# Kernel tuning notes

Measured on AMD Instinct MI355X. Metric: run time of the kernel, lower is better.

Reference implementation:

```python
import jax, jax.numpy as jnp
import numpy as np


def conv2d(x, w, pad):
    # x: [N,C,H,W], w: [O,I,kh,kw]
    return jax.lax.conv_general_dilated(
        x, w, window_strides=(1, 1), padding=[(pad, pad), (pad, pad)],
        dimension_numbers=("NCHW", "OIHW", "NCHW"))


def group_norm1(x, g, b, eps=1e-5):
    # GroupNorm(1, C): normalize over (C,H,W) per sample, per-channel affine
    mu = jnp.mean(x, axis=(1, 2, 3), keepdims=True)
    var = jnp.mean((x - mu) ** 2, axis=(1, 2, 3), keepdims=True)
    xn = (x - mu) * jax.lax.rsqrt(var + eps)
    return xn * g[None, :, None, None] + b[None, :, None, None]


def maxpool_3x3_s2(x):
    return jax.lax.reduce_window(
        x, -jnp.inf, jax.lax.max, (1, 1, 3, 3), (1, 1, 2, 2),
        ((0, 0), (0, 0), (1, 1), (1, 1)))


def hr2o_layer(x, wq, wk, wv, wo, g, b):
    # x: [N,C,H,W]; pairwise attention over the N ROIs at each (h,w)
    q = conv2d(x, wq, 1)
    k = conv2d(x, wk, 1)
    v = conv2d(x, wv, 1)
    scale = 1.0 / jnp.sqrt(jnp.asarray(x.shape[1], x.dtype))
    # torch: (q.unsqueeze(1) * k.unsqueeze(0)).sum(2) == einsum over channels
    att = jnp.einsum("nchw,mchw->nmhw", q, k) * scale  # [N,N,H,W]
    att = jax.nn.softmax(att, axis=1)                    # softmax over keys (dim=1)
    virt = jnp.einsum("nmhw,mchw->nchw", att, v)        # [N,C,H,W]
    virt = jax.nn.relu(group_norm1(virt, g, b))
    virt = conv2d(virt, wo, 1)
    return x + virt  # dropout is identity in eval mode


def setup_inputs() -> dict:
    key = jax.random.key(0)
    ks = jax.random.split(key, 12)
    N, C_R, H, W, HID, NCLS, DEPTH = 64, 1024, 16, 16, 512, 60, 2
    s = 0.02
    return {
        "bg_feats": jax.random.normal(ks[0], (C_R, H, W), jnp.float32),
        "actor_feats": jax.random.normal(ks[1], (N, C_R), jnp.float32),
        "w_conv1": jax.random.normal(ks[2], (HID, 2 * C_R, 1, 1), jnp.float32) * s,
        "w_conv2": jax.random.normal(ks[3], (HID, HID, 3, 3), jnp.float32) * s,
        "w_q": jax.random.normal(ks[4], (DEPTH, HID, HID, 3, 3), jnp.float32) * s,
        "w_k": jax.random.normal(ks[5], (DEPTH, HID, HID, 3, 3), jnp.float32) * s,
        "w_v": jax.random.normal(ks[6], (DEPTH, HID, HID, 3, 3), jnp.float32) * s,
        "w_o": jax.random.normal(ks[7], (DEPTH, HID, HID, 3, 3), jnp.float32) * s,
        "gamma": jnp.ones((DEPTH, HID), jnp.float32),
        "beta": jnp.zeros((DEPTH, HID), jnp.float32),
        "w_fc1": jax.random.normal(ks[8], (HID, C_R), jnp.float32) * s,
        "w_fc2": jax.random.normal(ks[9], (NCLS, 2 * HID), jnp.float32) * s,
    }


def reference(bg_feats, actor_feats, w_conv1, w_conv2, w_q, w_k, w_v, w_o,
              gamma, beta, w_fc1, w_fc2):
    N = actor_feats.shape[0]
    C_R, H, W = bg_feats.shape
    # bg repeated per ROI, actor features tiled over spatial dims
    bg = jnp.broadcast_to(bg_feats[None], (N, C_R, H, W))
    tiled = jnp.broadcast_to(actor_feats[:, :, None, None], (N, C_R, H, W))
    x = jnp.concatenate([bg, tiled], axis=1)           # [N, 2*C_R, H, W]
    x = jax.nn.relu(conv2d(x, w_conv1, 0))             # 1x1 -> [N,HID,H,W]
    x = jax.nn.relu(conv2d(x, w_conv2, 0))             # 3x3 pad=0 -> H-2,W-2
    x = maxpool_3x3_s2(x)                              # -> 7x7
    for d in range(w_q.shape[0]):
        x = hr2o_layer(x, w_q[d], w_k[d], w_v[d], w_o[d], gamma[d], beta[d])
    high_order = jnp.mean(x, axis=(2, 3))              # gap -> [N,HID]
    roi = jax.nn.relu(actor_feats @ w_fc1.T)           # [N,HID]
    out = jnp.concatenate([roi, high_order], axis=1) @ w_fc2.T  # [N,num_classes]
    return out
```

## Files before the change

kernel.cpp:

```cpp
#include <hip/hip_runtime.h>
#include <math.h>


typedef __bf16 bf16x8 __attribute__((ext_vector_type(8)));
typedef float  f32x4  __attribute__((ext_vector_type(4)));

#define NROI 64
#define CR   1024
#define HIDC 512
#define NCLS 60
#define PLANE (NROI * HIDC * 49)
#define ROWH 40
#define OCALL 4608
#define TAPSTR ((size_t)OCALL * 512)
#define WL (HIDC * HIDC * 9)
#define GNCNT 25088.0f

#if defined(__has_builtin)
#  if __has_builtin(__builtin_amdgcn_global_load_lds)
#    define HAVE_GLL 1
#  endif
#endif

__device__ __forceinline__ void stage16(const void* g, void* lds_base, int lane) {
#ifdef HAVE_GLL
    __builtin_amdgcn_global_load_lds(
        (const __attribute__((address_space(1))) unsigned int*)g,
        (__attribute__((address_space(3))) unsigned int*)lds_base, 16, 0, 0);
#else
    *(uint4*)((char*)lds_base + lane * 16) = *(const uint4*)g;
#endif
}

__device__ __forceinline__ float bf2f(unsigned short h) {
    union { unsigned u; float f; } x; x.u = (unsigned)h << 16; return x.f;
}

__global__ __launch_bounds__(256) void k_misc(
    const float* __restrict__ w2, const float* __restrict__ wq,
    const float* __restrict__ wk, const float* __restrict__ wv,
    const float* __restrict__ wo, const float* __restrict__ bg,
    __bf16* __restrict__ wAll, __bf16* __restrict__ inT7,
    __bf16* __restrict__ bgT)
{
    const int b = blockIdx.x, tid = threadIdx.x;
    if (b < 4608) {
        const int bid = b;
        const float* src;
        if (bid < 512) src = w2 + (size_t)bid * 4608;
        else if (bid < 2048) {
            const int r = bid - 512;
            const float* bb = r < 512 ? wq : (r < 1024 ? wk : wv);
            src = bb + (size_t)(r & 511) * 4608;
        } else if (bid < 2560) src = wo + (size_t)(bid - 2048) * 4608;
        else if (bid < 4096) {
            const int r = bid - 2560;
            const float* bb = r < 512 ? wq : (r < 1024 ? wk : wv);
            src = bb + WL + (size_t)(r & 511) * 4608;
        } else src = wo + WL + (size_t)(bid - 4096) * 4608;
        __shared__ float s[4608];
        const float4* s4 = (const float4*)src;
        for (int i = tid; i < 1152; i += 256) ((float4*)s)[i] = s4[i];
        __syncthreads();
        unsigned* dst = (unsigned*)wAll;
        const int c = tid * 2;
        const int swz = ((c >> 3) & 3) ^ ((bid >> 1) & 3);
        const size_t cidx = (size_t)(c >> 5) * 32 + swz * 8 + (c & 7);
#pragma unroll
        for (int t = 0; t < 9; ++t) {
            const unsigned short u0 = __builtin_bit_cast(unsigned short, (__bf16)s[c * 9 + t]);
            const unsigned short u1 = __builtin_bit_cast(unsigned short, (__bf16)s[(c + 1) * 9 + t]);
            dst[((size_t)t * TAPSTR + (size_t)bid * 512 + cidx) / 2] =
                ((unsigned)u1 << 16) | u0;
        }
    } else if (b < 5120) {
        const int k = b - 4608;
        const int n = k >> 3;
        const int j0 = (k & 7) * 4;
#pragma unroll
        for (int i = 0; i < 4; ++i) {
            const int jj = j0 + i;
            int sp;
            if (jj < 9) sp = jj;
            else if (jj < 18) sp = 63 + jj;
            else { const int t = jj - 18; sp = (1 + (t >> 1)) * 9 + (t & 1) * 8; }
            unsigned* d = (unsigned*)(inT7 + ((size_t)n * 81 + sp) * 512);
            d[tid] = 0u;
        }
    } else {
        const int cb = (b - 5120) * 8;
        const int p = tid;
        bf16x8 v;
#pragma unroll
        for (int j = 0; j < 8; ++j)
            v[j] = (__bf16)bg[(size_t)(cb + j) * 256 + p];
        *(bf16x8*)(bgT + (size_t)p * 1024 + cb) = v;
    }
}

__global__ __launch_bounds__(256, 2) void k_ab(
    const __bf16* __restrict__ bgT, const float* __restrict__ actor,
    const float* __restrict__ w1, const float* __restrict__ wfc1,
    float* __restrict__ A_T, float* __restrict__ Bp, float* __restrict__ roi)
{
    const int bx = blockIdx.x, by = blockIdx.y;
    const bool isA = bx < 4;
    const bool isRoi = (bx == 5);
    const int ocWg = by * 64;
    const int tid = threadIdx.x;
    const int w = tid >> 6, lane = tid & 63;
    const int q = lane >> 4, l16 = lane & 15;

    __shared__ __align__(16) __bf16 s_a[64 * ROWH];
    __shared__ __align__(16) __bf16 s_b[64 * ROWH];

    f32x4 acc[4];
#pragma unroll
    for (int nt = 0; nt < 4; ++nt) acc[nt] = (f32x4){0.f, 0.f, 0.f, 0.f};

    const int row = tid >> 2, part = tid & 3;
    for (int ch = 0; ch < 32; ++ch) {
        const int c0 = ch * 32;
        __syncthreads();
        if (isA) {
            const uint4 vv = *(const uint4*)(
                bgT + (size_t)(bx * 64 + row) * 1024 + c0 + part * 8);
            *(uint4*)(&s_a[row * ROWH + part * 8]) = vv;
        } else {
            const float* src = actor + (size_t)row * CR + c0 + part * 8;
            bf16x8 val;
#pragma unroll
            for (int j = 0; j < 8; ++j) val[j] = (__bf16)src[j];
            *(bf16x8*)(&s_a[row * ROWH + part * 8]) = val;
        }
        {
            const float* srcb = isRoi
                ? (wfc1 + (size_t)(ocWg + row) * CR + c0 + part * 8)
                : (w1 + (size_t)(ocWg + row) * (2 * CR)
                      + (isA ? 0 : CR) + c0 + part * 8);
            bf16x8 vb;
#pragma unroll
            for (int j = 0; j < 8; ++j) vb[j] = (__bf16)srcb[j];
            *(bf16x8*)(&s_b[row * ROWH + part * 8]) = vb;
        }
        __syncthreads();
        const bf16x8 af = *(const bf16x8*)(&s_a[(w * 16 + l16) * ROWH + q * 8]);
#pragma unroll
        for (int nt = 0; nt < 4; ++nt) {
            const bf16x8 bw = *(const bf16x8*)(&s_b[(nt * 16 + l16) * ROWH + q * 8]);
            acc[nt] = __builtin_amdgcn_mfma_f32_16x16x32_bf16(af, bw, acc[nt], 0, 0, 0);
        }
    }
#pragma unroll
    for (int r = 0; r < 4; ++r) {
#pragma unroll
        for (int nt = 0; nt < 4; ++nt) {
            const int mrow = w * 16 + q * 4 + r;
            const int oc = ocWg + nt * 16 + l16;
            if (isA)       A_T[(size_t)(bx * 64 + mrow) * 512 + oc] = acc[nt][r];
            else if (isRoi) roi[(size_t)mrow * 512 + oc] = fmaxf(acc[nt][r], 0.f);
            else           Bp[(size_t)mrow * 512 + oc] = acc[nt][r];
        }
    }
}

__global__ __launch_bounds__(256) void k_prep_in2(
    const float* __restrict__ A_T, const float* __restrict__ B,
    __bf16* __restrict__ dst)
{
    const int vn = blockIdx.x;
    const int n = vn >> 2, quad = vn & 3;
    const int sp0 = blockIdx.y * 27;
    const float b0 = B[n * HIDC + threadIdx.x];
    const float b1 = B[n * HIDC + 256 + threadIdx.x];
    for (int sp = sp0; sp < sp0 + 27; ++sp) {
        const int r = sp / 9, w = sp % 9;
        const int p16 = ((quad >> 1) * 7 + r) * 16 + (quad & 1) * 7 + w;
        __bf16* d = dst + ((size_t)vn * 81 + sp) * 512;
        d[threadIdx.x]       = (__bf16)fmaxf(A_T[p16 * HIDC + threadIdx.x] + b0, 0.f);
        d[256 + threadIdx.x] = (__bf16)fmaxf(A_T[p16 * HIDC + 256 + threadIdx.x] + b1, 0.f);
    }
}

template<int VN, int MODE>
__global__ __launch_bounds__(256, (VN == 4) ? 2 : 3) void k_conv_pipe(
    const __bf16* __restrict__ inT,
    const __bf16* __restrict__ wAll, int ocBaseGl,
    __bf16* __restrict__ outb,
    float* __restrict__ zeroStats, float* __restrict__ gapZero)
{
    constexpr int MT = (VN == 4) ? 4 : 2;
    constexpr int SLOTS = VN * 324;
    constexpr int NSUB = (SLOTS + 255) / 256;
    constexpr int SBUF = NSUB * 256;
    constexpr int NI = NSUB / 3;
    const int tid = threadIdx.x;
    const int w = tid >> 6, lane = tid & 63;
    const int q = lane >> 4, l16 = lane & 15;
    const int vn_l = (VN == 4) ? w : (w & 1);
    const int mh   = (VN == 4) ? 0 : (w >> 1);
    const int vnBase = blockIdx.x * VN;
    const int ocWg = blockIdx.y * 64;

    if (zeroStats && blockIdx.x == 0 && blockIdx.y == 0 && tid < 128)
        zeroStats[tid] = 0.f;
    if (gapZero && blockIdx.y == 0 && blockIdx.x < 16) {
        const float4 z = {0.f, 0.f, 0.f, 0.f};
        ((float4*)gapZero)[blockIdx.x * 512 + tid * 2]     = z;
        ((float4*)gapZero)[blockIdx.x * 512 + tid * 2 + 1] = z;
    }

    __shared__ __align__(16) __bf16 s_w[2 * 3 * 2048];
    __shared__ __align__(16) __bf16 s_in[2 * SBUF * 8];

    unsigned iGo[NSUB];
#pragma unroll
    for (int s = 0; s < NSUB; ++s) {
        int idx = tid + s * 256;
        if (idx > SLOTS - 1) idx = SLOTS - 1;
        const int vnl = idx / 324, rem = idx - vnl * 324;
        const int r = rem >> 2, part = rem & 3;
        iGo[s] = (unsigned)(((vnBase + vnl) * 81 + r) * 512
                            + ((part ^ (r & 3)) * 8));
    }
    const unsigned wGo = (unsigned)((ocBaseGl + ocWg + (tid >> 2)) * 512
                                    + (tid & 3) * 8);
    const int bOff = l16 * 32 + ((q ^ ((l16 >> 1) & 3)) << 3);

    int aLoc[MT];
#pragma unroll
    for (int mt = 0; mt < MT; ++mt) {
        int p = (mh * MT + mt) * 16 + l16;
        p = p > 48 ? 48 : p;
        aLoc[mt] = (p / 7) * 9 + (p % 7);
    }
    const int vb81 = vn_l * 81;

    f32x4 acc[MT][4];
#pragma unroll
    for (int a = 0; a < MT; ++a)
#pragma unroll
        for (int b = 0; b < 4; ++b) acc[a][b] = (f32x4){0.f, 0.f, 0.f, 0.f};

#pragma unroll
    for (int s = 0; s < NSUB; ++s)
        stage16(inT + iGo[s],
                (char*)s_in + (size_t)(s * 256 + w * 64) * 16, lane);
#pragma unroll
    for (int j = 0; j < 3; ++j)
        stage16(wAll + (size_t)j * TAPSTR + wGo,
                (char*)s_w + (size_t)j * 4096 + (size_t)w * 1024, lane);
    __syncthreads();

    for (int ch = 0; ch < 16; ++ch) {
        const int c0 = ch * 32;
        const int cur = ch & 1;
        const int nxt = cur ^ 1;
#pragma unroll
        for (int f = 0; f < 3; ++f) {
            const int P = ch * 3 + f;
            const int wpar = P & 1;
            {
                const int fn = (f == 2) ? 0 : (f + 1);
                const int cc = (f == 2) ? (c0 + 32) : c0;
#pragma unroll
                for (int j = 0; j < 3; ++j)
                    stage16(wAll + (size_t)(fn * 3 + j) * TAPSTR + wGo + cc,
                            (char*)s_w + (size_t)((wpar ^ 1) * 3 + j) * 4096
                                        + (size_t)w * 1024, lane);
            }
#pragma unroll
            for (int u = 0; u < NI; ++u) {
                const int s = f * NI + u;
                stage16(inT + iGo[s] + c0 + 32,
                        (char*)s_in + (size_t)nxt * (SBUF * 16)
                                    + (size_t)(s * 256 + w * 64) * 16, lane);
            }
            if (f == 0) {
                if constexpr (NI == 2) asm volatile("s_waitcnt vmcnt(5)" ::: "memory");
                else                   asm volatile("s_waitcnt vmcnt(4)" ::: "memory");
            } else {
                if constexpr (NI == 2) asm volatile("s_waitcnt vmcnt(7)" ::: "memory");
                else                   asm volatile("s_waitcnt vmcnt(5)" ::: "memory");
            }
            __builtin_amdgcn_sched_barrier(0);
            __builtin_amdgcn_s_barrier();
            __builtin_amdgcn_sched_barrier(0);
#pragma unroll
            for (int j = 0; j < 3; ++j) {
                const int DT = f * 9 + j;
                bf16x8 bw[4];
#pragma unroll
                for (int nt = 0; nt < 4; ++nt)
                    bw[nt] = *(const bf16x8*)(
                        &s_w[(wpar * 3 + j) * 2048 + nt * 512 + bOff]);
                bf16x8 af[MT];
#pragma unroll
                for (int mt = 0; mt < MT; ++mt) {
                    const int rl = aLoc[mt] + DT;
                    const int col = (q ^ (rl & 3)) << 3;
                    af[mt] = *(const bf16x8*)(
                        &s_in[cur * (SBUF * 8) + (vb81 + rl) * 32 + col]);
                }
#pragma unroll
                for (int mt = 0; mt < MT; ++mt)
#pragma unroll
                    for (int nt = 0; nt < 4; ++nt)
                        acc[mt][nt] = __builtin_amdgcn_mfma_f32_16x16x32_bf16(
                            af[mt], bw[nt], acc[mt][nt], 0, 0, 0);
            }
            __builtin_amdgcn_sched_barrier(0);
            __builtin_amdgcn_s_barrier();
        }
    }

    const int vn = vnBase + vn_l;
#pragma unroll
    for (int mt = 0; mt < MT; ++mt) {
#pragma unroll
        for (int r = 0; r < 4; ++r) {
            const int p = (mh * MT + mt) * 16 + q * 4 + r;
            if (p >= 49) continue;
#pragma unroll
            for (int nt = 0; nt < 4; ++nt) {
                const int oc = ocWg + nt * 16 + l16;
                const float v = acc[mt][nt][r];
                if (MODE == 2) {
                    const int n = vn >> 2, quad = vn & 3;
                    const int p14 = ((quad >> 1) * 7 + p / 7) * 14 + (quad & 1) * 7 + p % 7;
                    outb[((size_t)n * 196 + p14) * 512 + oc] = (__bf16)fmaxf(v, 0.f);
                } else {
                    const int conv = oc >> 9;
                    outb[(size_t)conv * PLANE + ((size_t)p * 64 + vn) * 512 + (oc & 511)]
                        = (__bf16)v;
                }
            }
        }
    }
}

template<int VN, bool GNIN>
__global__ __launch_bounds__(256, 2) void k_conv_mfma(
    const __bf16* __restrict__ inT,
    const float* __restrict__ vin,
    const float* __restrict__ statsRaw,
    const float* __restrict__ gamma, const float* __restrict__ beta,
    const __bf16* __restrict__ wAll, int ocBaseGl,
    const float* __restrict__ resid, float* __restrict__ outf,
    __bf16* __restrict__ outb, __bf16* __restrict__ inT7out,
    float* __restrict__ zeroStats, float* __restrict__ gapOut,
    float* __restrict__ gapZero, int mode)
{
    constexpr int MT = (VN == 4) ? 4 : ((VN == 2) ? 2 : 1);
    const int tid = threadIdx.x;
    const int w = tid >> 6, lane = tid & 63;
    const int q = lane >> 4, l16 = lane & 15;
    const int vn_l = (VN == 4) ? w : ((VN == 2) ? (w & 1) : 0);
    const int mh   = (VN == 4) ? 0 : ((VN == 2) ? (w >> 1) : w);
    const int vnBase = blockIdx.x * VN;
    const int ocWg = blockIdx.y * 64;

    if (zeroStats && blockIdx.x == 0 && blockIdx.y == 0 && tid < 128)
        zeroStats[tid] = 0.f;
    if (gapZero && blockIdx.y == 0 && blockIdx.x < 16) {
        const float4 z = {0.f, 0.f, 0.f, 0.f};
        ((float4*)gapZero)[blockIdx.x * 512 + tid * 2]     = z;
        ((float4*)gapZero)[blockIdx.x * 512 + tid * 2 + 1] = z;
    }

    __shared__ __align__(16) __bf16 s_w[9 * 64 * 32];
    __shared__ __align__(16) __bf16 s_in[VN * 81 * ROWH];
    __shared__ float s_mi[VN][2];
    __shared__ float s_gb[GNIN ? 1024 : 4];

    if (GNIN) {
        for (int k = tid; k < 512; k += 256) {
            s_gb[k]       = gamma[k];
            s_gb[512 + k] = beta[k];
        }
        if (tid < VN) {
            const float S = statsRaw[(vnBase + tid) * 2];
            const float Q = statsRaw[(vnBase + tid) * 2 + 1];
            const float mean = S / GNCNT;
            const float var  = Q / GNCNT - mean * mean;
            s_mi[tid][0] = mean;
            s_mi[tid][1] = rsqrtf(var + 1e-5f);
        }
    }

    const int bSwz = (q ^ ((l16 >> 1) & 3)) << 3;
    int aBase[MT];
#pragma unroll
    for (int mt = 0; mt < MT; ++mt) {
        int p = (mh * MT + mt) * 16 + l16;
        p = p > 48 ? 48 : p;
        aBase[mt] = (vn_l * 81 + (p / 7) * 9 + (p % 7)) * ROWH + q * 8;
    }

    f32x4 acc[MT][4];
#pragma unroll
    for (int a = 0; a < MT; ++a)
#pragma unroll
        for (int b = 0; b < 4; ++b) acc[a][b] = (f32x4){0.f, 0.f, 0.f, 0.f};

    for (int ch = 0; ch < 16; ++ch) {
        const int c0 = ch * 32;
        __syncthreads();
#pragma unroll
        for (int i = 0; i < 9; ++i) {
            const int s0 = (w * 9 + i) * 64;
            const int s = s0 + lane;
            const int t = s >> 8;
            const int rem = s & 255;
            const int row = rem >> 2, part = rem & 3;
            const __bf16* g = wAll + (size_t)t * TAPSTR
                + (size_t)(ocBaseGl + ocWg + row) * 512 + c0 + part * 8;
            stage16(g, (char*)s_w + (size_t)s0 * 16, lane);
        }
        for (int idx = tid; idx < VN * 324; idx += 256) {
            const int vnl = idx / 324, rem = idx - vnl * 324;
            const int r = rem >> 2, part = rem & 3;
            if (GNIN) {
                const int rr = r / 9, cc = r % 9;
                bf16x8 val;
                if (rr >= 1 && rr <= 7 && cc >= 1 && cc <= 7) {
                    const int p = (rr - 1) * 7 + (cc - 1);
                    const float* src = vin +
                        ((size_t)(vnBase + vnl) * 49 + p) * 512 + c0 + part * 8;
                    const float m = s_mi[vnl][0], iv = s_mi[vnl][1];
#pragma unroll
                    for (int j = 0; j < 8; ++j)
                        val[j] = (__bf16)fmaxf(
                            (src[j] - m) * iv * s_gb[c0 + part * 8 + j]
                            + s_gb[512 + c0 + part * 8 + j], 0.f);
                } else {
#pragma unroll
                    for (int j = 0; j < 8; ++j) val[j] = (__bf16)0.f;
                }
                *(bf16x8*)(&s_in[(vnl * 81 + r) * ROWH + part * 8]) = val;
            } else {
                const uint4 vv = *(const uint4*)(
                    inT + ((size_t)(vnBase + vnl) * 81 + r) * 512 + c0 + part * 8);
                *(uint4*)(&s_in[(vnl * 81 + r) * ROWH + part * 8]) = vv;
            }
        }
        __syncthreads();
#pragma unroll
        for (int t = 0; t < 9; ++t) {
            const int tOffA = ((t / 3) * 9 + (t % 3)) * ROWH;
            bf16x8 bw[4];
#pragma unroll
            for (int nt = 0; nt < 4; ++nt)
                bw[nt] = *(const bf16x8*)(&s_w[(t * 64 + nt * 16 + l16) * 32 + bSwz]);
            bf16x8 af[MT];
#pragma unroll
            for (int mt = 0; mt < MT; ++mt)
                af[mt] = *(const bf16x8*)(&s_in[aBase[mt] + tOffA]);
#pragma unroll
            for (int mt = 0; mt < MT; ++mt)
#pragma unroll
                for (int nt = 0; nt < 4; ++nt)
                    acc[mt][nt] = __builtin_amdgcn_mfma_f32_16x16x32_bf16(
                        af[mt], bw[nt], acc[mt][nt], 0, 0, 0);
        }
    }

    const int vn = vnBase + vn_l;
    float gsum[4] = {0.f, 0.f, 0.f, 0.f};
#pragma unroll
    for (int mt = 0; mt < MT; ++mt) {
#pragma unroll
        for (int r = 0; r < 4; ++r) {
            const int p = (mh * MT + mt) * 16 + q * 4 + r;
            if (p >= 49) continue;
#pragma unroll
            for (int nt = 0; nt < 4; ++nt) {
                const int oc = ocWg + nt * 16 + l16;
                const float v = acc[mt][nt][r];
                if (mode == 2) {
                    const int n = vn >> 2, quad = vn & 3;
                    const int p14 = ((quad >> 1) * 7 + p / 7) * 14 + (quad & 1) * 7 + p % 7;
                    outb[((size_t)n * 196 + p14) * 512 + oc] = (__bf16)fmaxf(v, 0.f);
                } else if (mode == 1) {
                    const size_t addr = ((size_t)vn * 49 + p) * 512 + oc;
                    const float res = v + resid[addr];
                    if (!gapOut) outf[addr] = res;
                    gsum[nt] += res;
                    if (inT7out) {
                        const int sp = (p / 7 + 1) * 9 + (p % 7 + 1);
                        inT7out[((size_t)vn * 81 + sp) * 512 + oc] = (__bf16)res;
                    }
                } else {
                    const int conv = oc >> 9;
                    outb[(size_t)conv * PLANE + ((size_t)p * 64 + vn) * 512 + (oc & 511)]
                        = (__bf16)v;
                }
            }
        }
    }
    if (gapOut) {
#pragma unroll
        for (int nt = 0; nt < 4; ++nt)
            atomicAdd(gapOut + (size_t)vn * 512 + ocWg + nt * 16 + l16, gsum[nt]);
    }
}

__global__ __launch_bounds__(256) void k_pool_prep(
    const __bf16* __restrict__ x2, __bf16* __restrict__ inT7,
    float* __restrict__ xA)
{
    const int b = blockIdx.x;
    const int n = b / 49, p = b % 49;
    const int i = p / 7, j = p % 7;
    const int sp = (i + 1) * 9 + (j + 1);
#pragma unroll
    for (int k = 0; k < 2; ++k) {
        const int c = threadIdx.x + k * 256;
        float mx = -1e30f;
#pragma unroll
        for (int di = -1; di <= 1; ++di) {
            const int rr = 2 * i + di;
            if (rr < 0 || rr >= 14) continue;
#pragma unroll
            for (int dj = -1; dj <= 1; ++dj) {
                const int cc = 2 * j + dj;
                if (cc < 0 || cc >= 14) continue;
                mx = fmaxf(mx, (float)x2[((size_t)n * 196 + rr * 14 + cc) * 512 + c]);
            }
        }
        inT7[((size_t)n * 81 + sp) * 512 + c] = (__bf16)mx;
        xA[((size_t)n * 49 + p) * 512 + c] = mx;
    }
}

__global__ __launch_bounds__(256) void k_attvirt(
    const __bf16* __restrict__ qT, const __bf16* __restrict__ kT,
    const __bf16* __restrict__ vT, float* __restrict__ virt,
    float* __restrict__ statsRaw)
{
    const int p = blockIdx.y;
    const int w = threadIdx.x >> 6, m = threadIdx.x & 63;
    const int n = blockIdx.x * 4 + w;
    __shared__ float s_q[4][HIDC];
    __shared__ float s_a[4][64];
    {
        const uint4 v = ((const uint4*)(qT + ((size_t)p * 64 + n) * HIDC))[m];
        const unsigned* u = (const unsigned*)&v;
#pragma unroll
        for (int j = 0; j < 4; ++j) {
            s_q[w][m * 8 + 2 * j]     = bf2f((unsigned short)(u[j] & 0xffff));
            s_q[w][m * 8 + 2 * j + 1] = bf2f((unsigned short)(u[j] >> 16));
        }
    }
    __syncthreads();
    const uint4* krow = (const uint4*)(kT + ((size_t)p * 64 + m) * HIDC);
    float acc0 = 0.f, acc1 = 0.f;
    for (int i = 0; i < 64; ++i) {
        const uint4 v = krow[i];
        const unsigned* u = (const unsigned*)&v;
#pragma unroll
        for (int j = 0; j < 2; ++j) {
            acc0 = fmaf(s_q[w][i * 8 + 2 * j],     bf2f((unsigned short)(u[j] & 0xffff)), acc0);
            acc0 = fmaf(s_q[w][i * 8 + 2 * j + 1], bf2f((unsigned short)(u[j] >> 16)),    acc0);
        }
#pragma unroll
        for (int j = 2; j < 4; ++j) {
            acc1 = fmaf(s_q[w][i * 8 + 2 * j],     bf2f((unsigned short)(u[j] & 0xffff)), acc1);
            acc1 = fmaf(s_q[w][i * 8 + 2 * j + 1], bf2f((unsigned short)(u[j] >> 16)),    acc1);
        }
    }
    float acc = (acc0 + acc1) * 0.044194173824159216f;
    float mx = acc;
#pragma unroll
    for (int off = 32; off; off >>= 1) mx = fmaxf(mx, __shfl_xor(mx, off));
    const float e = expf(acc - mx);
    float s = e;
#pragma unroll
    for (int off = 32; off; off >>= 1) s += __shfl_xor(s, off);
    s_a[w][m] = e / s;
    __syncthreads();
    const int c0 = m * 8;
    float av[8];
#pragma unroll
    for (int j = 0; j < 8; ++j) av[j] = 0.f;
    for (int mm = 0; mm < 64; ++mm) {
        const float a = s_a[w][mm];
        const uint4 v = *(const uint4*)(vT + ((size_t)p * 64 + mm) * HIDC + c0);
        const unsigned* u = (const unsigned*)&v;
#pragma unroll
        for (int j = 0; j < 4; ++j) {
            av[2 * j]     = fmaf(a, bf2f((unsigned short)(u[j] & 0xffff)), av[2 * j]);
            av[2 * j + 1] = fmaf(a, bf2f((unsigned short)(u[j] >> 16)),    av[2 * j + 1]);
        }
    }
    float* o = virt + ((size_t)n * 49 + p) * 512 + c0;
    float ps = 0.f, pq = 0.f;
#pragma unroll
    for (int j = 0; j < 8; ++j) {
        o[j] = av[j];
        ps += av[j];
        pq = fmaf(av[j], av[j], pq);
    }
#pragma unroll
    for (int off = 32; off; off >>= 1) {
        ps += __shfl_xor(ps, off);
        pq += __shfl_xor(pq, off);
    }
    if (m == 0) {
        atomicAdd(statsRaw + n * 2, ps);
        atomicAdd(statsRaw + n * 2 + 1, pq);
    }
}

__global__ __launch_bounds__(256) void k_final(
    const float* __restrict__ roi, const float* __restrict__ gap,
    const float* __restrict__ wfc2, float* __restrict__ out)
{
    const int n = blockIdx.x, tid = threadIdx.x;
    __shared__ float s[1024];
    s[tid]       = roi[(size_t)n * 512 + tid];
    s[tid + 256] = roi[(size_t)n * 512 + 256 + tid];
    s[tid + 512] = gap[(size_t)n * 512 + tid] * (1.f / 49.f);
    s[tid + 768] = gap[(size_t)n * 512 + 256 + tid] * (1.f / 49.f);
    __syncthreads();
    if (tid < 240) {
        const int k = tid >> 2, part = tid & 3;
        const float4* w4 = (const float4*)(wfc2 + (size_t)k * 1024 + part * 256);
        const float4* s4 = (const float4*)(s + part * 256);
        float a0 = 0.f, a1 = 0.f, a2 = 0.f, a3 = 0.f;
        for (int i = 0; i < 64; ++i) {
            const float4 wv = w4[i], sv = s4[i];
            a0 = fmaf(wv.x, sv.x, a0); a1 = fmaf(wv.y, sv.y, a1);
            a2 = fmaf(wv.z, sv.z, a2); a3 = fmaf(wv.w, sv.w, a3);
        }
        float acc = (a0 + a1) + (a2 + a3);
        acc += __shfl_xor(acc, 1);
        acc += __shfl_xor(acc, 2);
        if (part == 0) out[n * NCLS + k] = acc;
    }
}

extern "C" void kernel_launch(void* const* d_in, const int* in_sizes, int n_in,
                              void* d_out, int out_size, void* d_ws, size_t ws_size,
                              hipStream_t stream) {
    const float* bg    = (const float*)d_in[0];
    const float* actor = (const float*)d_in[1];
    const float* w1    = (const float*)d_in[2];
    const float* w2    = (const float*)d_in[3];
    const float* wq    = (const float*)d_in[4];
    const float* wk    = (const float*)d_in[5];
    const float* wv    = (const float*)d_in[6];
    const float* wo    = (const float*)d_in[7];
    const float* gamma = (const float*)d_in[8];
    const float* beta  = (const float*)d_in[9];
    const float* wfc1  = (const float*)d_in[10];
    const float* wfc2  = (const float*)d_in[11];
    float* out = (float*)d_out;
    float* ws  = (float*)d_ws;

    float* A_T   = ws;
    float* Bp    = A_T + 131072;
    float* xA    = Bp + 32768;
    float* xB    = xA + PLANE;
    float* stats = xB + PLANE;
    float* roi   = stats + 128;
    float* gap   = roi + 32768;
    float* fend  = gap + 32768;
    __bf16* x2h  = (__bf16*)fend;
    float*  virt = (float*)x2h;
    __bf16* inT2 = x2h + 6422528;
    __bf16* qkvT = inT2;
    __bf16* inT7 = inT2 + 10616832;
    __bf16* wAll = inT7 + 2654208;
    __bf16* bgT  = wAll + (size_t)9 * OCALL * 512;

    k_misc<<<5248, 256, 0, stream>>>(w2, wq, wk, wv, wo, bg, wAll, inT7, bgT);
    k_ab<<<dim3(6, 8), 256, 0, stream>>>(bgT, actor, w1, wfc1, A_T, Bp, roi);
    k_prep_in2<<<dim3(256, 3), 256, 0, stream>>>(A_T, Bp, inT2);
    k_conv_pipe<4, 2><<<dim3(64, 8), 256, 0, stream>>>(
        inT2, wAll, 0, x2h, nullptr, nullptr);
    k_pool_prep<<<64 * 49, 256, 0, stream>>>(x2h, inT7, xA);

    float* xin = xA;
    float* xout = xB;
    for (int d = 0; d < 2; ++d) {
        k_conv_pipe<2, 0><<<dim3(32, 24), 256, 0, stream>>>(
            inT7, wAll, 512 + d * 2048, qkvT, stats,
            d == 1 ? gap : nullptr);
        k_attvirt<<<dim3(16, 49), 256, 0, stream>>>(
            qkvT, qkvT + PLANE, qkvT + 2 * PLANE, virt, stats);
        k_conv_mfma<1, true><<<dim3(64, 8), 256, 0, stream>>>(
            nullptr, virt, stats, gamma + d * HIDC, beta + d * HIDC,
            wAll, 2048 + d * 2048, xin, xout, nullptr,
            d == 0 ? inT7 : nullptr, nullptr,
            d == 1 ? gap : nullptr, nullptr, 1);
        float* t = xin; xin = xout; xout = t;
    }
    k_final<<<64, 256, 0, stream>>>(roi, gap, wfc2, out);
}
```

Measured before the change: 602.0 us.

## Split GroupNorm prep into its own kernel and run output conv on pipelined path

The output convolution used to apply GroupNorm, affine and ReLU while staging its input on every channel chunk, inside a non-pipelined MFMA kernel. Now a separate kernel writes the normalized, zero-padded bf16 activations once. The output conv then runs through the software-pipelined k_conv_pipe kernel, which gains a residual/GAP epilogue mode. The cost is an extra launch and an extra round trip of the bf16 activations through global memory. The output conv grid also shrinks from 512 to 256 blocks.

```diff
diff --git a/kernel.cpp b/kernel.cpp
--- a/kernel.cpp
+++ b/kernel.cpp
@@ -182,12 +182,48 @@
     }
 }
 
+__global__ __launch_bounds__(256) void k_prep_gn(
+    const float* __restrict__ virt, const float* __restrict__ statsRaw,
+    const float* __restrict__ gamma, const float* __restrict__ beta,
+    __bf16* __restrict__ gnT)
+{
+    const int vn = blockIdx.x;
+    const int sp0 = blockIdx.y * 9;
+    __shared__ float s_mi[2];
+    if (threadIdx.x == 0) {
+        const float S = statsRaw[vn * 2], Q = statsRaw[vn * 2 + 1];
+        const float mean = S / GNCNT;
+        s_mi[0] = mean;
+        s_mi[1] = rsqrtf(Q / GNCNT - mean * mean + 1e-5f);
+    }
+    __syncthreads();
+    const float m = s_mi[0], iv = s_mi[1];
+    const int c0 = threadIdx.x, c1 = threadIdx.x + 256;
+    const float g0 = gamma[c0], g1 = gamma[c1];
+    const float b0 = beta[c0],  b1 = beta[c1];
+    for (int sp = sp0; sp < sp0 + 9; ++sp) {
+        const int rr = sp / 9, cc = sp % 9;
+        __bf16* d = gnT + ((size_t)vn * 81 + sp) * 512;
+        if (rr >= 1 && rr <= 7 && cc >= 1 && cc <= 7) {
+            const int p = (rr - 1) * 7 + (cc - 1);
+            const float* src = virt + ((size_t)vn * 49 + p) * 512;
+            d[c0] = (__bf16)fmaxf((src[c0] - m) * iv * g0 + b0, 0.f);
+            d[c1] = (__bf16)fmaxf((src[c1] - m) * iv * g1 + b1, 0.f);
+        } else {
+            d[c0] = (__bf16)0.f;
+            d[c1] = (__bf16)0.f;
+        }
+    }
+}
+
 template<int VN, int MODE>
 __global__ __launch_bounds__(256, (VN == 4) ? 2 : 3) void k_conv_pipe(
     const __bf16* __restrict__ inT,
     const __bf16* __restrict__ wAll, int ocBaseGl,
     __bf16* __restrict__ outb,
-    float* __restrict__ zeroStats, float* __restrict__ gapZero)
+    float* __restrict__ zeroStats, float* __restrict__ gapZero,
+    const float* __restrict__ resid, float* __restrict__ outf,
+    __bf16* __restrict__ inT7out, float* __restrict__ gapOut)
 {
     constexpr int MT = (VN == 4) ? 4 : 2;
     constexpr int SLOTS = VN * 324;
@@ -315,6 +351,7 @@
     }
 
     const int vn = vnBase + vn_l;
+    float gsum[4] = {0.f, 0.f, 0.f, 0.f};
 #pragma unroll
     for (int mt = 0; mt < MT; ++mt) {
 #pragma unroll
@@ -325,163 +362,11 @@
             for (int nt = 0; nt < 4; ++nt) {
                 const int oc = ocWg + nt * 16 + l16;
                 const float v = acc[mt][nt][r];
-                if (MODE == 2) {
+                if constexpr (MODE == 2) {
                     const int n = vn >> 2, quad = vn & 3;
                     const int p14 = ((quad >> 1) * 7 + p / 7) * 14 + (quad & 1) * 7 + p % 7;
                     outb[((size_t)n * 196 + p14) * 512 + oc] = (__bf16)fmaxf(v, 0.f);
-                } else {
-                    const int conv = oc >> 9;
-                    outb[(size_t)conv * PLANE + ((size_t)p * 64 + vn) * 512 + (oc & 511)]
-                        = (__bf16)v;
-                }
-            }
-        }
-    }
-}
-
-template<int VN, bool GNIN>
-__global__ __launch_bounds__(256, 2) void k_conv_mfma(
-    const __bf16* __restrict__ inT,
-    const float* __restrict__ vin,
-    const float* __restrict__ statsRaw,
-    const float* __restrict__ gamma, const float* __restrict__ beta,
-    const __bf16* __restrict__ wAll, int ocBaseGl,
-    const float* __restrict__ resid, float* __restrict__ outf,
-    __bf16* __restrict__ outb, __bf16* __restrict__ inT7out,
-    float* __restrict__ zeroStats, float* __restrict__ gapOut,
-    float* __restrict__ gapZero, int mode)
-{
-    constexpr int MT = (VN == 4) ? 4 : ((VN == 2) ? 2 : 1);
-    const int tid = threadIdx.x;
-    const int w = tid >> 6, lane = tid & 63;
-    const int q = lane >> 4, l16 = lane & 15;
-    const int vn_l = (VN == 4) ? w : ((VN == 2) ? (w & 1) : 0);
-    const int mh   = (VN == 4) ? 0 : ((VN == 2) ? (w >> 1) : w);
-    const int vnBase = blockIdx.x * VN;
-    const int ocWg = blockIdx.y * 64;
-
-    if (zeroStats && blockIdx.x == 0 && blockIdx.y == 0 && tid < 128)
-        zeroStats[tid] = 0.f;
-    if (gapZero && blockIdx.y == 0 && blockIdx.x < 16) {
-        const float4 z = {0.f, 0.f, 0.f, 0.f};
-        ((float4*)gapZero)[blockIdx.x * 512 + tid * 2]     = z;
-        ((float4*)gapZero)[blockIdx.x * 512 + tid * 2 + 1] = z;
-    }
-
-    __shared__ __align__(16) __bf16 s_w[9 * 64 * 32];
-    __shared__ __align__(16) __bf16 s_in[VN * 81 * ROWH];
-    __shared__ float s_mi[VN][2];
-    __shared__ float s_gb[GNIN ? 1024 : 4];
-
-    if (GNIN) {
-        for (int k = tid; k < 512; k += 256) {
-            s_gb[k]       = gamma[k];
-            s_gb[512 + k] = beta[k];
-        }
-        if (tid < VN) {
-            const float S = statsRaw[(vnBase + tid) * 2];
-            const float Q = statsRaw[(vnBase + tid) * 2 + 1];
-            const float mean = S / GNCNT;
-            const float var  = Q / GNCNT - mean * mean;
-            s_mi[tid][0] = mean;
-            s_mi[tid][1] = rsqrtf(var + 1e-5f);
-        }
-    }
-
-    const int bSwz = (q ^ ((l16 >> 1) & 3)) << 3;
-    int aBase[MT];
-#pragma unroll
-    for (int mt = 0; mt < MT; ++mt) {
-        int p = (mh * MT + mt) * 16 + l16;
-        p = p > 48 ? 48 : p;
-        aBase[mt] = (vn_l * 81 + (p / 7) * 9 + (p % 7)) * ROWH + q * 8;
-    }
-
-    f32x4 acc[MT][4];
-#pragma unroll
-    for (int a = 0; a < MT; ++a)
-#pragma unroll
-        for (int b = 0; b < 4; ++b) acc[a][b] = (f32x4){0.f, 0.f, 0.f, 0.f};
-
-    for (int ch = 0; ch < 16; ++ch) {
-        const int c0 = ch * 32;
-        __syncthreads();
-#pragma unroll
-        for (int i = 0; i < 9; ++i) {
-            const int s0 = (w * 9 + i) * 64;
-            const int s = s0 + lane;
-            const int t = s >> 8;
-            const int rem = s & 255;
-            const int row = rem >> 2, part = rem & 3;
-            const __bf16* g = wAll + (size_t)t * TAPSTR
-                + (size_t)(ocBaseGl + ocWg + row) * 512 + c0 + part * 8;
-            stage16(g, (char*)s_w + (size_t)s0 * 16, lane);
-        }
-        for (int idx = tid; idx < VN * 324; idx += 256) {
-            const int vnl = idx / 324, rem = idx - vnl * 324;
-            const int r = rem >> 2, part = rem & 3;
-            if (GNIN) {
-                const int rr = r / 9, cc = r % 9;
-                bf16x8 val;
-                if (rr >= 1 && rr <= 7 && cc >= 1 && cc <= 7) {
-                    const int p = (rr - 1) * 7 + (cc - 1);
-                    const float* src = vin +
-                        ((size_t)(vnBase + vnl) * 49 + p) * 512 + c0 + part * 8;
-                    const float m = s_mi[vnl][0], iv = s_mi[vnl][1];
-#pragma unroll
-                    for (int j = 0; j < 8; ++j)
-                        val[j] = (__bf16)fmaxf(
-                            (src[j] - m) * iv * s_gb[c0 + part * 8 + j]
-                            + s_gb[512 + c0 + part * 8 + j], 0.f);
-                } else {
-#pragma unroll
-                    for (int j = 0; j < 8; ++j) val[j] = (__bf16)0.f;
-                }
-                *(bf16x8*)(&s_in[(vnl * 81 + r) * ROWH + part * 8]) = val;
-            } else {
-                const uint4 vv = *(const uint4*)(
-                    inT + ((size_t)(vnBase + vnl) * 81 + r) * 512 + c0 + part * 8);
-                *(uint4*)(&s_in[(vnl * 81 + r) * ROWH + part * 8]) = vv;
-            }
-        }
-        __syncthreads();
-#pragma unroll
-        for (int t = 0; t < 9; ++t) {
-            const int tOffA = ((t / 3) * 9 + (t % 3)) * ROWH;
-            bf16x8 bw[4];
-#pragma unroll
-            for (int nt = 0; nt < 4; ++nt)
-                bw[nt] = *(const bf16x8*)(&s_w[(t * 64 + nt * 16 + l16) * 32 + bSwz]);
-            bf16x8 af[MT];
-#pragma unroll
-            for (int mt = 0; mt < MT; ++mt)
-                af[mt] = *(const bf16x8*)(&s_in[aBase[mt] + tOffA]);
-#pragma unroll
-            for (int mt = 0; mt < MT; ++mt)
-#pragma unroll
-                for (int nt = 0; nt < 4; ++nt)
-                    acc[mt][nt] = __builtin_amdgcn_mfma_f32_16x16x32_bf16(
-                        af[mt], bw[nt], acc[mt][nt], 0, 0, 0);
-        }
-    }
-
-    const int vn = vnBase + vn_l;
-    float gsum[4] = {0.f, 0.f, 0.f, 0.f};
-#pragma unroll
-    for (int mt = 0; mt < MT; ++mt) {
-#pragma unroll
-        for (int r = 0; r < 4; ++r) {
-            const int p = (mh * MT + mt) * 16 + q * 4 + r;
-            if (p >= 49) continue;
-#pragma unroll
-            for (int nt = 0; nt < 4; ++nt) {
-                const int oc = ocWg + nt * 16 + l16;
-                const float v = acc[mt][nt][r];
-                if (mode == 2) {
-                    const int n = vn >> 2, quad = vn & 3;
-                    const int p14 = ((quad >> 1) * 7 + p / 7) * 14 + (quad & 1) * 7 + p % 7;
-                    outb[((size_t)n * 196 + p14) * 512 + oc] = (__bf16)fmaxf(v, 0.f);
-                } else if (mode == 1) {
+                } else if constexpr (MODE == 1) {
                     const size_t addr = ((size_t)vn * 49 + p) * 512 + oc;
                     const float res = v + resid[addr];
                     if (!gapOut) outf[addr] = res;
@@ -498,10 +383,12 @@
             }
         }
     }
-    if (gapOut) {
-#pragma unroll
-        for (int nt = 0; nt < 4; ++nt)
-            atomicAdd(gapOut + (size_t)vn * 512 + ocWg + nt * 16 + l16, gsum[nt]);
+    if constexpr (MODE == 1) {
+        if (gapOut) {
+#pragma unroll
+            for (int nt = 0; nt < 4; ++nt)
+                atomicAdd(gapOut + (size_t)vn * 512 + ocWg + nt * 16 + l16, gsum[nt]);
+        }
     }
 }
 
@@ -673,12 +560,14 @@
     __bf16* inT7 = inT2 + 10616832;
     __bf16* wAll = inT7 + 2654208;
     __bf16* bgT  = wAll + (size_t)9 * OCALL * 512;
+    __bf16* gnT  = bgT + 262144;
 
     k_misc<<<5248, 256, 0, stream>>>(w2, wq, wk, wv, wo, bg, wAll, inT7, bgT);
     k_ab<<<dim3(6, 8), 256, 0, stream>>>(bgT, actor, w1, wfc1, A_T, Bp, roi);
     k_prep_in2<<<dim3(256, 3), 256, 0, stream>>>(A_T, Bp, inT2);
     k_conv_pipe<4, 2><<<dim3(64, 8), 256, 0, stream>>>(
-        inT2, wAll, 0, x2h, nullptr, nullptr);
+        inT2, wAll, 0, x2h, nullptr, nullptr,
+        nullptr, nullptr, nullptr, nullptr);
     k_pool_prep<<<64 * 49, 256, 0, stream>>>(x2h, inT7, xA);
 
     float* xin = xA;
@@ -686,14 +575,15 @@
     for (int d = 0; d < 2; ++d) {
         k_conv_pipe<2, 0><<<dim3(32, 24), 256, 0, stream>>>(
             inT7, wAll, 512 + d * 2048, qkvT, stats,
-            d == 1 ? gap : nullptr);
+            d == 1 ? gap : nullptr,
+            nullptr, nullptr, nullptr, nullptr);
         k_attvirt<<<dim3(16, 49), 256, 0, stream>>>(
             qkvT, qkvT + PLANE, qkvT + 2 * PLANE, virt, stats);
-        k_conv_mfma<1, true><<<dim3(64, 8), 256, 0, stream>>>(
-            nullptr, virt, stats, gamma + d * HIDC, beta + d * HIDC,
-            wAll, 2048 + d * 2048, xin, xout, nullptr,
-            d == 0 ? inT7 : nullptr, nullptr,
-            d == 1 ? gap : nullptr, nullptr, 1);
+        k_prep_gn<<<dim3(64, 9), 256, 0, stream>>>(
+            virt, stats, gamma + d * HIDC, beta + d * HIDC, gnT);
+        k_conv_pipe<2, 1><<<dim3(32, 8), 256, 0, stream>>>(
+            gnT, wAll, 2048 + d * 2048, nullptr, nullptr, nullptr,
+            xin, xout, d == 0 ? inT7 : nullptr, d == 1 ? gap : nullptr);
         float* t = xin; xin = xout; xout = t;
     }
     k_final<<<64, 256, 0, stream>>>(roi, gap, wfc2, out);
```

After: 592.5 us, median of 2. No clear change (-1.6%).
